# Performance work log

Hardware: AMD Instinct MI355X
Metric: run time of the kernel (lower is better)

The kernel has to match this reference:

```python
import jax, jax.numpy as jnp
import numpy as np

B, S, DIM = 2, 2048, 1024
H = 16
HD = DIM // H  # 64
SCALE = HD ** -0.5


def setup_inputs() -> dict:
    key = jax.random.key(0)
    k1, k2, k3 = jax.random.split(key, 3)
    x = jax.random.normal(k1, (B, S, DIM), dtype=jnp.float32)
    # Linear weights scaled ~1/sqrt(fan_in) like torch default init
    Wqkv = jax.random.normal(k2, (DIM, 3 * DIM), dtype=jnp.float32) * (DIM ** -0.5)
    Wproj = jax.random.normal(k3, (DIM, DIM), dtype=jnp.float32) * (DIM ** -0.5)
    return {"x": x, "Wqkv": Wqkv, "Wproj": Wproj}


def reference(x, Wqkv, Wproj):
    Bsz, Slen, dim = x.shape
    qkv = x @ Wqkv  # (B, S, 3*dim)
    qkv = qkv.reshape(Bsz, Slen, 3, H, HD)
    q, k, v = qkv[:, :, 0], qkv[:, :, 1], qkv[:, :, 2]  # each (B, S, H, HD)
    # softmax attention (chunking in the original is memory-only; math identical)
    scores = jnp.einsum("bshd,bthd->bhst", q, k) * SCALE  # (B, H, S, S)
    attn = jax.nn.softmax(scores, axis=-1)
    out = jnp.einsum("bhst,bthd->bshd", attn, v)  # (B, S, H, HD)
    out = out.reshape(Bsz, Slen, dim)
    return out @ Wproj
```

## Files before the change

kernel.cpp:

```cpp
#include <hip/hip_runtime.h>
#include <stdint.h>

typedef unsigned short u16;
typedef __attribute__((ext_vector_type(8))) short bf16x8;
typedef __attribute__((ext_vector_type(4))) float f32x4;

#define BATCH 2
#define SEQ 2048
#define NH 16
#define HDIM 64
#define DMODEL 1024
#define MTOT (BATCH * SEQ)
#define QKV_N (3 * DMODEL)
#define ATT_SCALE 0.125f
#define L2E 1.44269504088896340736f
#define C2 (ATT_SCALE * L2E)

#define BAR() asm volatile("s_barrier" ::: "memory")

__device__ __forceinline__ u16 f2b(float f) {
    uint32_t x = __builtin_bit_cast(uint32_t, f);
    uint32_t r = (x + 0x7fffu + ((x >> 16) & 1u)) >> 16;
    return (u16)r;
}

__device__ __forceinline__ uint32_t cvt_pk(float lo, float hi) {
    uint32_t r;
    asm("v_cvt_pk_bf16_f32 %0, %1, %2" : "=v"(r) : "v"(lo), "v"(hi));
    return r;
}

__device__ __forceinline__ void gl_lds16(const void* g, void* l) {
    __builtin_amdgcn_global_load_lds(
        (const __attribute__((address_space(1))) void*)g,
        (__attribute__((address_space(3))) void*)l, 16, 0, 0);
}

__global__ __launch_bounds__(256) void k_cvt(const float* __restrict__ in,
                                             u16* __restrict__ out, int n8) {
    int i = blockIdx.x * blockDim.x + threadIdx.x;
    if (i >= n8) return;
    const float4* p = (const float4*)in + (size_t)i * 2;
    float4 a = p[0], b = p[1];
    union { uint32_t w[4]; uint4 v; } u;
    u.w[0] = cvt_pk(a.x, a.y);
    u.w[1] = cvt_pk(a.z, a.w);
    u.w[2] = cvt_pk(b.x, b.y);
    u.w[3] = cvt_pk(b.z, b.w);
    *(uint4*)(out + (size_t)i * 8) = u.v;
}

__global__ __launch_bounds__(256) void k_wtrans(const float* __restrict__ W,
                                                u16* __restrict__ WT,
                                                int rows, int cols) {
    __shared__ float tile[64][65];
    const int c0 = blockIdx.x * 64, r0 = blockIdx.y * 64;
    const int tx = threadIdx.x & 63, ty = threadIdx.x >> 6;
#pragma unroll
    for (int i = 0; i < 16; ++i) {
        int r = i * 4 + ty;
        tile[r][tx] = W[(size_t)(r0 + r) * cols + c0 + tx];
    }
    __syncthreads();
#pragma unroll
    for (int i = 0; i < 16; ++i) {
        int c = i * 4 + ty;
        WT[(size_t)(c0 + c) * rows + r0 + tx] = f2b(tile[tx][c]);
    }
}

__global__ __launch_bounds__(512, 2) void k_gemm_qkv8(const u16* __restrict__ A,
                                                      const u16* __restrict__ BT,
                                                      u16* __restrict__ C) {
    extern __shared__ __align__(16) u16 lds[];
    const int tid = threadIdx.x, wid = tid >> 6, lane = tid & 63;
    const int r = lane & 15, g = lane >> 4;
    const int wr = wid >> 2, wc = wid & 3;
    const int m0 = blockIdx.y * 256, n0 = blockIdx.x * 256;
    const int K = DMODEL;

    auto STG = [&](int kt2, int rg) {
        const int isB = rg >> 1, half = rg & 1;
        const u16* src = isB ? BT : A;
        const int rowb = (isB ? n0 : m0) + half * 128 + wid * 16 + (lane >> 2);
        const u16* s = src + (size_t)rowb * K + kt2 * 64 + (lane & 3) * 8;
        const int dst = (kt2 & 1) * 32768 + isB * 16384 + half * 8192 +
                        wid * 1024 + lane * 8;
        gl_lds16(s, &lds[dst]);
        gl_lds16(s + 32, &lds[dst + 512]);
    };

    f32x4 acc[8][4] = {};
    bf16x8 a[4][2], b[4][2];
    const int aB = wr * 8192 + r * 32 + g * 8;
    const int bB = 16384 + (wc >> 1) * 8192 + (wc & 1) * 4096 + r * 32 + g * 8;

#pragma unroll
    for (int t2 = 0; t2 < 2; ++t2)
#pragma unroll
        for (int rg = 0; rg < 4; ++rg) STG(t2, rg);
    asm volatile("s_waitcnt vmcnt(0)" ::: "memory");
    __syncthreads();

    for (int kt = 0; kt < 16; ++kt) {
        const int sb = (kt & 1) * 32768;
#pragma unroll
        for (int mi = 0; mi < 4; ++mi)
#pragma unroll
            for (int kk = 0; kk < 2; ++kk)
                a[mi][kk] = *(const bf16x8*)&lds[sb + aB + (mi * 2 + kk) * 512];
#pragma unroll
        for (int ni = 0; ni < 2; ++ni)
#pragma unroll
            for (int kk = 0; kk < 2; ++kk)
                b[ni][kk] = *(const bf16x8*)&lds[sb + bB + (ni * 2 + kk) * 512];
        BAR();
        __builtin_amdgcn_s_setprio(1);
#pragma unroll
        for (int mi = 0; mi < 4; ++mi)
#pragma unroll
            for (int ni = 0; ni < 2; ++ni)
#pragma unroll
                for (int kk = 0; kk < 2; ++kk)
                    acc[mi][ni] = __builtin_amdgcn_mfma_f32_16x16x32_bf16(
                        b[ni][kk], a[mi][kk], acc[mi][ni], 0, 0, 0);
        __builtin_amdgcn_s_setprio(0);
        BAR();
#pragma unroll
        for (int ni = 2; ni < 4; ++ni)
#pragma unroll
            for (int kk = 0; kk < 2; ++kk)
                b[ni][kk] = *(const bf16x8*)&lds[sb + bB + (ni * 2 + kk) * 512];
        BAR();
        __builtin_amdgcn_s_setprio(1);
#pragma unroll
        for (int mi = 0; mi < 4; ++mi)
#pragma unroll
            for (int ni = 2; ni < 4; ++ni)
#pragma unroll
                for (int kk = 0; kk < 2; ++kk)
                    acc[mi][ni] = __builtin_amdgcn_mfma_f32_16x16x32_bf16(
                        b[ni][kk], a[mi][kk], acc[mi][ni], 0, 0, 0);
        __builtin_amdgcn_s_setprio(0);
        BAR();
#pragma unroll
        for (int mi = 0; mi < 4; ++mi)
#pragma unroll
            for (int kk = 0; kk < 2; ++kk)
                a[mi][kk] = *(const bf16x8*)&lds[sb + aB + ((4 + mi) * 2 + kk) * 512];
        if (kt < 14) { STG(kt + 2, 2); STG(kt + 2, 3); }
        BAR();
        __builtin_amdgcn_s_setprio(1);
#pragma unroll
        for (int mi = 0; mi < 4; ++mi)
#pragma unroll
            for (int ni = 2; ni < 4; ++ni)
#pragma unroll
                for (int kk = 0; kk < 2; ++kk)
                    acc[4 + mi][ni] = __builtin_amdgcn_mfma_f32_16x16x32_bf16(
                        b[ni][kk], a[mi][kk], acc[4 + mi][ni], 0, 0, 0);
        __builtin_amdgcn_s_setprio(0);
        BAR();
        if (kt < 14) { STG(kt + 2, 0); STG(kt + 2, 1); }
        BAR();
        __builtin_amdgcn_s_setprio(1);
#pragma unroll
        for (int mi = 0; mi < 4; ++mi)
#pragma unroll
            for (int ni = 0; ni < 2; ++ni)
#pragma unroll
                for (int kk = 0; kk < 2; ++kk)
                    acc[4 + mi][ni] = __builtin_amdgcn_mfma_f32_16x16x32_bf16(
                        b[ni][kk], a[mi][kk], acc[4 + mi][ni], 0, 0, 0);
        __builtin_amdgcn_s_setprio(0);
        if (kt < 14) {
            asm volatile("s_waitcnt vmcnt(8)" ::: "memory");
        } else if (kt == 14) {
            asm volatile("s_waitcnt vmcnt(0)" ::: "memory");
        }
        BAR();
    }

#pragma unroll
    for (int mi = 0; mi < 8; ++mi)
#pragma unroll
        for (int ni = 0; ni < 4; ++ni) {
            const int row = m0 + wr * 128 + mi * 16 + r;
            const int col = n0 + wc * 64 + ni * 16 + g * 4;
            union { uint32_t w[2]; ushort4 v; } o;
            o.w[0] = cvt_pk(acc[mi][ni][0], acc[mi][ni][1]);
            o.w[1] = cvt_pk(acc[mi][ni][2], acc[mi][ni][3]);
            *(ushort4*)&C[(size_t)row * QKV_N + col] = o.v;
        }
}

template <bool F32OUT>
__global__ __launch_bounds__(256) void k_gemm_bt(const u16* __restrict__ A,
                                                 const u16* __restrict__ BT,
                                                 void* __restrict__ C,
                                                 int M, int N, int K) {
    __shared__ __align__(16) u16 As[128 * 64];
    __shared__ __align__(16) u16 Bs[128 * 64];
    const int tid = threadIdx.x;
    const int wid = tid >> 6, lane = tid & 63;
    const int r = lane & 15, g = lane >> 4;
    const int m0 = blockIdx.y * 128, n0 = blockIdx.x * 128;
    const int wm = (wid >> 1) * 64, wn = (wid & 1) * 64;
    const int srow = lane >> 3, scol = (lane & 7) * 8;
    f32x4 acc[4][4] = {};
    for (int k0 = 0; k0 < K; k0 += 64) {
#pragma unroll
        for (int i = 0; i < 4; ++i) {
            const int li = wid * 4 + i;
            gl_lds16(A + (size_t)(m0 + li * 8 + srow) * K + k0 + scol, &As[li * 512]);
            gl_lds16(BT + (size_t)(n0 + li * 8 + srow) * K + k0 + scol, &Bs[li * 512]);
        }
        __syncthreads();
#pragma unroll
        for (int kk = 0; kk < 2; ++kk) {
            bf16x8 af[4], bfr[4];
#pragma unroll
            for (int mi = 0; mi < 4; ++mi)
                af[mi] = *(const bf16x8*)&As[(wm + mi * 16 + r) * 64 + kk * 32 + g * 8];
#pragma unroll
            for (int ni = 0; ni < 4; ++ni)
                bfr[ni] = *(const bf16x8*)&Bs[(wn + ni * 16 + r) * 64 + kk * 32 + g * 8];
#pragma unroll
            for (int mi = 0; mi < 4; ++mi)
#pragma unroll
                for (int ni = 0; ni < 4; ++ni)
                    acc[mi][ni] = __builtin_amdgcn_mfma_f32_16x16x32_bf16(
                        bfr[ni], af[mi], acc[mi][ni], 0, 0, 0);
        }
        __syncthreads();
    }
#pragma unroll
    for (int mi = 0; mi < 4; ++mi)
#pragma unroll
        for (int ni = 0; ni < 4; ++ni) {
            const int row = m0 + wm + mi * 16 + r;
            const int col = n0 + wn + ni * 16 + g * 4;
            if (F32OUT) {
                float4 vv;
                vv.x = acc[mi][ni][0]; vv.y = acc[mi][ni][1];
                vv.z = acc[mi][ni][2]; vv.w = acc[mi][ni][3];
                *(float4*)&((float*)C)[(size_t)row * N + col] = vv;
            } else {
                union { uint32_t w[2]; ushort4 v; } o;
                o.w[0] = cvt_pk(acc[mi][ni][0], acc[mi][ni][1]);
                o.w[1] = cvt_pk(acc[mi][ni][2], acc[mi][ni][3]);
                *(ushort4*)&((u16*)C)[(size_t)row * N + col] = o.v;
            }
        }
}

__global__ __launch_bounds__(256) void k_vtrans(const u16* __restrict__ qkv,
                                                u16* __restrict__ Vt) {
    __shared__ u16 tile[64][65];
    const int bh = blockIdx.y;
    const int b = bh >> 4, h = bh & 15;
    const int s0 = blockIdx.x * 64;
    const int tx = threadIdx.x & 63, ty = threadIdx.x >> 6;
#pragma unroll
    for (int i = 0; i < 16; ++i) {
        int s = i * 4 + ty;
        tile[s][tx] = qkv[(size_t)(b * SEQ + s0 + s) * QKV_N + 2 * DMODEL + h * HDIM + tx];
    }
    __syncthreads();
#pragma unroll
    for (int i = 0; i < 16; ++i) {
        int hd = i * 4 + ty;
        Vt[((size_t)bh * HDIM + hd) * SEQ + s0 + tx] = tile[tx][hd];
    }
}

__global__ __launch_bounds__(256) void k_attn(const u16* __restrict__ qkv,
                                              const u16* __restrict__ Vt,
                                              u16* __restrict__ O) {
    __shared__ __align__(16) u16 Ks[2][4096];
    __shared__ __align__(16) u16 Vs[2][4096];
    const int bh = blockIdx.y;
    const int b = bh >> 4, h = bh & 15;
    const int q0 = blockIdx.x * 64;
    const int tid = threadIdx.x, wid = tid >> 6, lane = tid & 63;
    const int r = lane & 15, g = lane >> 4;

    const size_t qbase = (size_t)(b * SEQ + q0 + wid * 16 + r) * QKV_N + h * HDIM;
    const bf16x8 qf0 = *(const bf16x8*)&qkv[qbase + g * 8];
    const bf16x8 qf1 = *(const bf16x8*)&qkv[qbase + 32 + g * 8];

    float mL = -1e30f, lsum = 0.f;
    f32x4 oacc[4] = {};
    const int kc0 = wid * 2;

#define STAGE(BUF, SK0)                                                          \
    {                                                                            \
        _Pragma("unroll") for (int i = 0; i < 2; ++i) {                          \
            const int kc = kc0 + i;                                              \
            const int ksrow = (kc >> 2) * 32 + g * 8 + (kc & 1) * 4 + ((lane >> 2) & 3); \
            const int kscol = ((kc >> 1) & 1) * 32 + (lane & 3) * 8;             \
            gl_lds16(&qkv[(size_t)(b * SEQ + (SK0) + ksrow) * QKV_N + DMODEL +   \
                          h * HDIM + kscol],                                     \
                     &Ks[BUF][kc * 512]);                                        \
            const int vhd = (kc & 3) * 16 + r;                                   \
            const int vsc = (kc >> 2) * 32 + g * 8;                              \
            gl_lds16(&Vt[((size_t)bh * HDIM + vhd) * SEQ + (SK0) + vsc],         \
                     &Vs[BUF][kc * 512]);                                        \
        }                                                                        \
    }

    STAGE(0, 0);
    asm volatile("s_waitcnt vmcnt(0)");
    __syncthreads();

    for (int t = 0; t < SEQ / 64; ++t) {
        const int cur = t & 1;
        if (t < SEQ / 64 - 1) STAGE(cur ^ 1, (t + 1) * 64);

        f32x4 sacc[4] = {};
        __builtin_amdgcn_s_setprio(1);
#pragma unroll
        for (int nf = 0; nf < 4; ++nf) {
            const int kbase = (nf & 1) * 2048 + (nf >> 1) * 512 +
                              (r >> 2) * 128 + (r & 3) * 32 + g * 8;
            bf16x8 kf0 = *(const bf16x8*)&Ks[cur][kbase];
            bf16x8 kf1 = *(const bf16x8*)&Ks[cur][kbase + 1024];
            sacc[nf] = __builtin_amdgcn_mfma_f32_16x16x32_bf16(kf0, qf0, sacc[nf], 0, 0, 0);
            sacc[nf] = __builtin_amdgcn_mfma_f32_16x16x32_bf16(kf1, qf1, sacc[nf], 0, 0, 0);
        }
        __builtin_amdgcn_s_setprio(0);

        float m0a = fmaxf(fmaxf(sacc[0][0], sacc[0][1]), fmaxf(sacc[0][2], sacc[0][3]));
        float m1a = fmaxf(fmaxf(sacc[1][0], sacc[1][1]), fmaxf(sacc[1][2], sacc[1][3]));
        float m2a = fmaxf(fmaxf(sacc[2][0], sacc[2][1]), fmaxf(sacc[2][2], sacc[2][3]));
        float m3a = fmaxf(fmaxf(sacc[3][0], sacc[3][1]), fmaxf(sacc[3][2], sacc[3][3]));
        const float pm = fmaxf(fmaxf(m0a, m1a), fmaxf(m2a, m3a)) * C2;
        if (!__all(pm <= mL + 8.f)) {
            float rm = pm;
            rm = fmaxf(rm, __shfl_xor(rm, 16, 64));
            rm = fmaxf(rm, __shfl_xor(rm, 32, 64));
            const float mNew = fmaxf(mL, rm);
            const float al = exp2f(mL - mNew);
            mL = mNew;
            lsum *= al;
#pragma unroll
            for (int ht = 0; ht < 4; ++ht)
#pragma unroll
                for (int e = 0; e < 4; ++e) oacc[ht][e] *= al;
        }
        float p[4][4];
#pragma unroll
        for (int nf = 0; nf < 4; ++nf)
#pragma unroll
            for (int e = 0; e < 4; ++e) {
                p[nf][e] = exp2f(sacc[nf][e] * C2 - mL);
                lsum += p[nf][e];
            }

        union { uint32_t w[4]; bf16x8 v; } upf0, upf1;
        upf0.w[0] = cvt_pk(p[0][0], p[0][1]);
        upf0.w[1] = cvt_pk(p[0][2], p[0][3]);
        upf0.w[2] = cvt_pk(p[2][0], p[2][1]);
        upf0.w[3] = cvt_pk(p[2][2], p[2][3]);
        upf1.w[0] = cvt_pk(p[1][0], p[1][1]);
        upf1.w[1] = cvt_pk(p[1][2], p[1][3]);
        upf1.w[2] = cvt_pk(p[3][0], p[3][1]);
        upf1.w[3] = cvt_pk(p[3][2], p[3][3]);

        __builtin_amdgcn_s_setprio(1);
#pragma unroll
        for (int ht = 0; ht < 4; ++ht) {
            bf16x8 vf0 = *(const bf16x8*)&Vs[cur][ht * 512 + g * 128 + r * 8];
            bf16x8 vf1 = *(const bf16x8*)&Vs[cur][(4 + ht) * 512 + g * 128 + r * 8];
            oacc[ht] = __builtin_amdgcn_mfma_f32_16x16x32_bf16(vf0, upf0.v, oacc[ht], 0, 0, 0);
            oacc[ht] = __builtin_amdgcn_mfma_f32_16x16x32_bf16(vf1, upf1.v, oacc[ht], 0, 0, 0);
        }
        __builtin_amdgcn_s_setprio(0);

        asm volatile("s_waitcnt vmcnt(0)");
        __syncthreads();
    }
#undef STAGE

    lsum += __shfl_xor(lsum, 16, 64);
    lsum += __shfl_xor(lsum, 32, 64);
    const float inv = 1.0f / lsum;
    const size_t obase = (size_t)(b * SEQ + q0 + wid * 16 + r) * DMODEL + h * HDIM;
#pragma unroll
    for (int ht = 0; ht < 4; ++ht) {
        union { uint32_t w[2]; ushort4 v; } o;
        o.w[0] = cvt_pk(oacc[ht][0] * inv, oacc[ht][1] * inv);
        o.w[1] = cvt_pk(oacc[ht][2] * inv, oacc[ht][3] * inv);
        *(ushort4*)&O[obase + ht * 16 + g * 4] = o.v;
    }
}

extern "C" void kernel_launch(void* const* d_in, const int* in_sizes, int n_in,
                              void* d_out, int out_size, void* d_ws, size_t ws_size,
                              hipStream_t stream) {
    const float* x = (const float*)d_in[0];
    const float* Wqkv = (const float*)d_in[1];
    const float* Wproj = (const float*)d_in[2];
    float* out = (float*)d_out;

    u16* xb = (u16*)d_ws;
    u16* WqkvT = xb + (size_t)MTOT * DMODEL;
    u16* WprojT = WqkvT + (size_t)QKV_N * DMODEL;
    u16* qkv = WprojT + (size_t)DMODEL * DMODEL;
    u16* Vt = qkv + (size_t)MTOT * QKV_N;
    u16* Ob = Vt + (size_t)BATCH * NH * HDIM * SEQ;

    hipFuncSetAttribute(reinterpret_cast<const void*>(k_gemm_qkv8),
                        hipFuncAttributeMaxDynamicSharedMemorySize, 131072);

    k_cvt<<<dim3((MTOT * DMODEL / 8) / 256), 256, 0, stream>>>(x, xb, MTOT * DMODEL / 8);
    k_wtrans<<<dim3(QKV_N / 64, DMODEL / 64), 256, 0, stream>>>(Wqkv, WqkvT, DMODEL, QKV_N);
    k_wtrans<<<dim3(DMODEL / 64, DMODEL / 64), 256, 0, stream>>>(Wproj, WprojT, DMODEL, DMODEL);
    k_gemm_qkv8<<<dim3(QKV_N / 256, MTOT / 256), 512, 131072, stream>>>(xb, WqkvT, qkv);
    k_vtrans<<<dim3(SEQ / 64, BATCH * NH), 256, 0, stream>>>(qkv, Vt);
    k_attn<<<dim3(SEQ / 64, BATCH * NH), 256, 0, stream>>>(qkv, Vt, Ob);
    k_gemm_bt<true><<<dim3(DMODEL / 128, MTOT / 128), 256, 0, stream>>>(
        Ob, WprojT, (void*)out, MTOT, DMODEL, DMODEL);
}
```

Baseline: 230.3 us.

## Merge prep kernels, fuse V transpose into QKV GEMM, retile projection GEMM

Combines the x conversion and both weight transposes into one launch, and has the QKV GEMM epilogue write V directly in transposed layout, which removes the separate V transpose kernel. The projection GEMM uses a smaller 64x128 tile to get more blocks. The attention kernel switches to incrementing staging pointers and uses a three-input max chain. These changes aim to cut launch overhead and an extra pass over V, at the cost of scattered 2-byte stores in the V epilogue.

```diff
diff --git a/kernel.cpp b/kernel.cpp
--- a/kernel.cpp
+++ b/kernel.cpp
@@ -17,6 +17,7 @@
 #define C2 (ATT_SCALE * L2E)
 
 #define BAR() asm volatile("s_barrier" ::: "memory")
+#define F3(a, b, c) fmaxf(fmaxf((a), (b)), (c))
 
 __device__ __forceinline__ u16 f2b(float f) {
     uint32_t x = __builtin_bit_cast(uint32_t, f);
@@ -36,26 +37,39 @@
         (__attribute__((address_space(3))) void*)l, 16, 0, 0);
 }
 
-__global__ __launch_bounds__(256) void k_cvt(const float* __restrict__ in,
-                                             u16* __restrict__ out, int n8) {
-    int i = blockIdx.x * blockDim.x + threadIdx.x;
-    if (i >= n8) return;
-    const float4* p = (const float4*)in + (size_t)i * 2;
-    float4 a = p[0], b = p[1];
-    union { uint32_t w[4]; uint4 v; } u;
-    u.w[0] = cvt_pk(a.x, a.y);
-    u.w[1] = cvt_pk(a.z, a.w);
-    u.w[2] = cvt_pk(b.x, b.y);
-    u.w[3] = cvt_pk(b.z, b.w);
-    *(uint4*)(out + (size_t)i * 8) = u.v;
-}
-
-__global__ __launch_bounds__(256) void k_wtrans(const float* __restrict__ W,
-                                                u16* __restrict__ WT,
-                                                int rows, int cols) {
+__global__ __launch_bounds__(256) void k_prep(const float* __restrict__ x,
+                                              const float* __restrict__ Wq,
+                                              const float* __restrict__ Wp,
+                                              u16* __restrict__ xb,
+                                              u16* __restrict__ WqT,
+                                              u16* __restrict__ WpT) {
+    const int bid = blockIdx.x, tid = threadIdx.x;
+    if (bid < 2048) {
+        const int i = bid * 256 + tid;
+        const float4* p = (const float4*)x + (size_t)i * 2;
+        float4 a = p[0], b = p[1];
+        union { uint32_t w[4]; uint4 v; } u;
+        u.w[0] = cvt_pk(a.x, a.y);
+        u.w[1] = cvt_pk(a.z, a.w);
+        u.w[2] = cvt_pk(b.x, b.y);
+        u.w[3] = cvt_pk(b.z, b.w);
+        *(uint4*)(xb + (size_t)i * 8) = u.v;
+        return;
+    }
     __shared__ float tile[64][65];
-    const int c0 = blockIdx.x * 64, r0 = blockIdx.y * 64;
-    const int tx = threadIdx.x & 63, ty = threadIdx.x >> 6;
+    const float* W;
+    u16* WT;
+    int cols, bx, by;
+    if (bid < 2048 + 768) {
+        const int j = bid - 2048;
+        W = Wq; WT = WqT; cols = QKV_N; bx = j % 48; by = j / 48;
+    } else {
+        const int j = bid - 2816;
+        W = Wp; WT = WpT; cols = DMODEL; bx = j % 16; by = j / 16;
+    }
+    const int rows = DMODEL;
+    const int c0 = bx * 64, r0 = by * 64;
+    const int tx = tid & 63, ty = tid >> 6;
 #pragma unroll
     for (int i = 0; i < 16; ++i) {
         int r = i * 4 + ty;
@@ -71,7 +85,8 @@
 
 __global__ __launch_bounds__(512, 2) void k_gemm_qkv8(const u16* __restrict__ A,
                                                       const u16* __restrict__ BT,
-                                                      u16* __restrict__ C) {
+                                                      u16* __restrict__ C,
+                                                      u16* __restrict__ Vt) {
     extern __shared__ __align__(16) u16 lds[];
     const int tid = threadIdx.x, wid = tid >> 6, lane = tid & 63;
     const int r = lane & 15, g = lane >> 4;
@@ -181,54 +196,77 @@
         BAR();
     }
 
-#pragma unroll
-    for (int mi = 0; mi < 8; ++mi)
-#pragma unroll
-        for (int ni = 0; ni < 4; ++ni) {
-            const int row = m0 + wr * 128 + mi * 16 + r;
-            const int col = n0 + wc * 64 + ni * 16 + g * 4;
-            union { uint32_t w[2]; ushort4 v; } o;
-            o.w[0] = cvt_pk(acc[mi][ni][0], acc[mi][ni][1]);
-            o.w[1] = cvt_pk(acc[mi][ni][2], acc[mi][ni][3]);
-            *(ushort4*)&C[(size_t)row * QKV_N + col] = o.v;
-        }
-}
-
-template <bool F32OUT>
-__global__ __launch_bounds__(256) void k_gemm_bt(const u16* __restrict__ A,
-                                                 const u16* __restrict__ BT,
-                                                 void* __restrict__ C,
-                                                 int M, int N, int K) {
-    __shared__ __align__(16) u16 As[128 * 64];
+    if (n0 < 2 * DMODEL) {
+#pragma unroll
+        for (int mi = 0; mi < 8; ++mi)
+#pragma unroll
+            for (int ni = 0; ni < 4; ++ni) {
+                const int row = m0 + wr * 128 + mi * 16 + r;
+                const int col = n0 + wc * 64 + ni * 16 + g * 4;
+                union { uint32_t w[2]; ushort4 v; } o;
+                o.w[0] = cvt_pk(acc[mi][ni][0], acc[mi][ni][1]);
+                o.w[1] = cvt_pk(acc[mi][ni][2], acc[mi][ni][3]);
+                *(ushort4*)&C[(size_t)row * QKV_N + col] = o.v;
+            }
+    } else {
+        const int h_ = ((n0 - 2 * DMODEL) >> 6) + wc;
+#pragma unroll
+        for (int mi = 0; mi < 8; ++mi)
+#pragma unroll
+            for (int ni = 0; ni < 4; ++ni) {
+                const int row = m0 + wr * 128 + mi * 16 + r;
+                const int b_ = row >> 11, s_ = row & (SEQ - 1);
+                const int hd0 = ni * 16 + g * 4;
+                union { uint32_t w[2]; u16 t[4]; } o;
+                o.w[0] = cvt_pk(acc[mi][ni][0], acc[mi][ni][1]);
+                o.w[1] = cvt_pk(acc[mi][ni][2], acc[mi][ni][3]);
+                const size_t base =
+                    ((size_t)(b_ * NH + h_) * HDIM + hd0) * SEQ + s_;
+                Vt[base] = o.t[0];
+                Vt[base + SEQ] = o.t[1];
+                Vt[base + 2 * SEQ] = o.t[2];
+                Vt[base + 3 * SEQ] = o.t[3];
+            }
+    }
+}
+
+__global__ __launch_bounds__(256) void k_gemm_proj(const u16* __restrict__ A,
+                                                   const u16* __restrict__ BT,
+                                                   float* __restrict__ C) {
+    __shared__ __align__(16) u16 As[64 * 64];
     __shared__ __align__(16) u16 Bs[128 * 64];
     const int tid = threadIdx.x;
     const int wid = tid >> 6, lane = tid & 63;
     const int r = lane & 15, g = lane >> 4;
-    const int m0 = blockIdx.y * 128, n0 = blockIdx.x * 128;
-    const int wm = (wid >> 1) * 64, wn = (wid & 1) * 64;
+    const int m0 = blockIdx.y * 64, n0 = blockIdx.x * 128;
     const int srow = lane >> 3, scol = (lane & 7) * 8;
-    f32x4 acc[4][4] = {};
+    const int K = DMODEL;
+    f32x4 acc[4][2] = {};
     for (int k0 = 0; k0 < K; k0 += 64) {
+#pragma unroll
+        for (int i = 0; i < 2; ++i) {
+            const int li = wid * 2 + i;
+            gl_lds16(A + (size_t)(m0 + li * 8 + srow) * K + k0 + scol, &As[li * 512]);
+        }
 #pragma unroll
         for (int i = 0; i < 4; ++i) {
             const int li = wid * 4 + i;
-            gl_lds16(A + (size_t)(m0 + li * 8 + srow) * K + k0 + scol, &As[li * 512]);
             gl_lds16(BT + (size_t)(n0 + li * 8 + srow) * K + k0 + scol, &Bs[li * 512]);
         }
         __syncthreads();
 #pragma unroll
         for (int kk = 0; kk < 2; ++kk) {
-            bf16x8 af[4], bfr[4];
+            bf16x8 af[4], bfr[2];
 #pragma unroll
             for (int mi = 0; mi < 4; ++mi)
-                af[mi] = *(const bf16x8*)&As[(wm + mi * 16 + r) * 64 + kk * 32 + g * 8];
-#pragma unroll
-            for (int ni = 0; ni < 4; ++ni)
-                bfr[ni] = *(const bf16x8*)&Bs[(wn + ni * 16 + r) * 64 + kk * 32 + g * 8];
+                af[mi] = *(const bf16x8*)&As[(mi * 16 + r) * 64 + kk * 32 + g * 8];
+#pragma unroll
+            for (int ni = 0; ni < 2; ++ni)
+                bfr[ni] = *(const bf16x8*)&Bs[(wid * 32 + ni * 16 + r) * 64 + kk * 32 + g * 8];
 #pragma unroll
             for (int mi = 0; mi < 4; ++mi)
 #pragma unroll
-                for (int ni = 0; ni < 4; ++ni)
+                for (int ni = 0; ni < 2; ++ni)
                     acc[mi][ni] = __builtin_amdgcn_mfma_f32_16x16x32_bf16(
                         bfr[ni], af[mi], acc[mi][ni], 0, 0, 0);
         }
@@ -237,41 +275,14 @@
 #pragma unroll
     for (int mi = 0; mi < 4; ++mi)
 #pragma unroll
-        for (int ni = 0; ni < 4; ++ni) {
-            const int row = m0 + wm + mi * 16 + r;
-            const int col = n0 + wn + ni * 16 + g * 4;
-            if (F32OUT) {
-                float4 vv;
-                vv.x = acc[mi][ni][0]; vv.y = acc[mi][ni][1];
-                vv.z = acc[mi][ni][2]; vv.w = acc[mi][ni][3];
-                *(float4*)&((float*)C)[(size_t)row * N + col] = vv;
-            } else {
-                union { uint32_t w[2]; ushort4 v; } o;
-                o.w[0] = cvt_pk(acc[mi][ni][0], acc[mi][ni][1]);
-                o.w[1] = cvt_pk(acc[mi][ni][2], acc[mi][ni][3]);
-                *(ushort4*)&((u16*)C)[(size_t)row * N + col] = o.v;
-            }
-        }
-}
-
-__global__ __launch_bounds__(256) void k_vtrans(const u16* __restrict__ qkv,
-                                                u16* __restrict__ Vt) {
-    __shared__ u16 tile[64][65];
-    const int bh = blockIdx.y;
-    const int b = bh >> 4, h = bh & 15;
-    const int s0 = blockIdx.x * 64;
-    const int tx = threadIdx.x & 63, ty = threadIdx.x >> 6;
-#pragma unroll
-    for (int i = 0; i < 16; ++i) {
-        int s = i * 4 + ty;
-        tile[s][tx] = qkv[(size_t)(b * SEQ + s0 + s) * QKV_N + 2 * DMODEL + h * HDIM + tx];
-    }
-    __syncthreads();
-#pragma unroll
-    for (int i = 0; i < 16; ++i) {
-        int hd = i * 4 + ty;
-        Vt[((size_t)bh * HDIM + hd) * SEQ + s0 + tx] = tile[tx][hd];
-    }
+        for (int ni = 0; ni < 2; ++ni) {
+            const int row = m0 + mi * 16 + r;
+            const int col = n0 + wid * 32 + ni * 16 + g * 4;
+            float4 vv;
+            vv.x = acc[mi][ni][0]; vv.y = acc[mi][ni][1];
+            vv.z = acc[mi][ni][2]; vv.w = acc[mi][ni][3];
+            *(float4*)&C[(size_t)row * DMODEL + col] = vv;
+        }
 }
 
 __global__ __launch_bounds__(256) void k_attn(const u16* __restrict__ qkv,
@@ -293,29 +304,39 @@
     f32x4 oacc[4] = {};
     const int kc0 = wid * 2;
 
-#define STAGE(BUF, SK0)                                                          \
-    {                                                                            \
-        _Pragma("unroll") for (int i = 0; i < 2; ++i) {                          \
-            const int kc = kc0 + i;                                              \
-            const int ksrow = (kc >> 2) * 32 + g * 8 + (kc & 1) * 4 + ((lane >> 2) & 3); \
-            const int kscol = ((kc >> 1) & 1) * 32 + (lane & 3) * 8;             \
-            gl_lds16(&qkv[(size_t)(b * SEQ + (SK0) + ksrow) * QKV_N + DMODEL +   \
-                          h * HDIM + kscol],                                     \
-                     &Ks[BUF][kc * 512]);                                        \
-            const int vhd = (kc & 3) * 16 + r;                                   \
-            const int vsc = (kc >> 2) * 32 + g * 8;                              \
-            gl_lds16(&Vt[((size_t)bh * HDIM + vhd) * SEQ + (SK0) + vsc],         \
-                     &Vs[BUF][kc * 512]);                                        \
-        }                                                                        \
-    }
-
-    STAGE(0, 0);
+    const u16* kp[2];
+    const u16* vp[2];
+    int kdst[2], vdst[2];
+#pragma unroll
+    for (int i = 0; i < 2; ++i) {
+        const int kc = kc0 + i;
+        const int ksrow = (kc >> 2) * 32 + g * 8 + (kc & 1) * 4 + ((lane >> 2) & 3);
+        const int kscol = ((kc >> 1) & 1) * 32 + (lane & 3) * 8;
+        kp[i] = qkv + (size_t)(b * SEQ + ksrow) * QKV_N + DMODEL + h * HDIM + kscol;
+        const int vhd = (kc & 3) * 16 + r;
+        const int vsc = (kc >> 2) * 32 + g * 8;
+        vp[i] = Vt + ((size_t)bh * HDIM + vhd) * SEQ + vsc;
+        kdst[i] = kc * 512;
+        vdst[i] = kc * 512;
+    }
+
+#define STAGE(BUF)                                                   \
+    {                                                                \
+        _Pragma("unroll") for (int i = 0; i < 2; ++i) {              \
+            gl_lds16(kp[i], &Ks[BUF][kdst[i]]);                      \
+            gl_lds16(vp[i], &Vs[BUF][vdst[i]]);                      \
+            kp[i] += 64 * QKV_N;                                     \
+            vp[i] += 64;                                             \
+        }                                                            \
+    }
+
+    STAGE(0);
     asm volatile("s_waitcnt vmcnt(0)");
     __syncthreads();
 
     for (int t = 0; t < SEQ / 64; ++t) {
         const int cur = t & 1;
-        if (t < SEQ / 64 - 1) STAGE(cur ^ 1, (t + 1) * 64);
+        if (t < SEQ / 64 - 1) STAGE(cur ^ 1);
 
         f32x4 sacc[4] = {};
         __builtin_amdgcn_s_setprio(1);
@@ -330,11 +351,15 @@
         }
         __builtin_amdgcn_s_setprio(0);
 
-        float m0a = fmaxf(fmaxf(sacc[0][0], sacc[0][1]), fmaxf(sacc[0][2], sacc[0][3]));
-        float m1a = fmaxf(fmaxf(sacc[1][0], sacc[1][1]), fmaxf(sacc[1][2], sacc[1][3]));
-        float m2a = fmaxf(fmaxf(sacc[2][0], sacc[2][1]), fmaxf(sacc[2][2], sacc[2][3]));
-        float m3a = fmaxf(fmaxf(sacc[3][0], sacc[3][1]), fmaxf(sacc[3][2], sacc[3][3]));
-        const float pm = fmaxf(fmaxf(m0a, m1a), fmaxf(m2a, m3a)) * C2;
+        float mt = F3(sacc[0][0], sacc[0][1], sacc[0][2]);
+        mt = F3(mt, sacc[0][3], sacc[1][0]);
+        mt = F3(mt, sacc[1][1], sacc[1][2]);
+        mt = F3(mt, sacc[1][3], sacc[2][0]);
+        mt = F3(mt, sacc[2][1], sacc[2][2]);
+        mt = F3(mt, sacc[2][3], sacc[3][0]);
+        mt = F3(mt, sacc[3][1], sacc[3][2]);
+        mt = fmaxf(mt, sacc[3][3]);
+        const float pm = mt * C2;
         if (!__all(pm <= mL + 8.f)) {
             float rm = pm;
             rm = fmaxf(rm, __shfl_xor(rm, 16, 64));
@@ -413,12 +438,9 @@
     hipFuncSetAttribute(reinterpret_cast<const void*>(k_gemm_qkv8),
                         hipFuncAttributeMaxDynamicSharedMemorySize, 131072);
 
-    k_cvt<<<dim3((MTOT * DMODEL / 8) / 256), 256, 0, stream>>>(x, xb, MTOT * DMODEL / 8);
-    k_wtrans<<<dim3(QKV_N / 64, DMODEL / 64), 256, 0, stream>>>(Wqkv, WqkvT, DMODEL, QKV_N);
-    k_wtrans<<<dim3(DMODEL / 64, DMODEL / 64), 256, 0, stream>>>(Wproj, WprojT, DMODEL, DMODEL);
-    k_gemm_qkv8<<<dim3(QKV_N / 256, MTOT / 256), 512, 131072, stream>>>(xb, WqkvT, qkv);
-    k_vtrans<<<dim3(SEQ / 64, BATCH * NH), 256, 0, stream>>>(qkv, Vt);
+    k_prep<<<dim3(3072), 256, 0, stream>>>(x, Wqkv, Wproj, xb, WqkvT, WprojT);
+    k_gemm_qkv8<<<dim3(QKV_N / 256, MTOT / 256), 512, 131072, stream>>>(
+        xb, WqkvT, qkv, Vt);
     k_attn<<<dim3(SEQ / 64, BATCH * NH), 256, 0, stream>>>(qkv, Vt, Ob);
-    k_gemm_bt<true><<<dim3(DMODEL / 128, MTOT / 128), 256, 0, stream>>>(
-        Ob, WprojT, (void*)out, MTOT, DMODEL, DMODEL);
-}
+    k_gemm_proj<<<dim3(DMODEL / 128, MTOT / 64), 256, 0, stream>>>(Ob, WprojT, out);
+}
```

Measured after the change: 216.8 us. 1.06x faster.
